# Kernel tuning notes

Measured on AMD Instinct MI355X. Metric: run time of the kernel, lower is better.

Reference implementation:

```python
import jax, jax.numpy as jnp
import numpy as np

G = 2            # num codevector groups
C = 320          # codes per group
VQ_DIM = 256     # codevector_dim
D = VQ_DIM // G  # per-group code dim = 128
TAU = 2.0        # gumbel temperature


def setup_inputs() -> dict:
    key = jax.random.key(0)
    k1, k2, k3, k4, k5, k6 = jax.random.split(key, 6)
    B, T, H = 16, 3072, 512
    x = jax.random.normal(k1, (B, T, H), dtype=jnp.float32)
    masked_token_idx = jax.random.randint(k2, (B, T), 0, 2) > 0  # bool mask
    gumbel_noise = jax.random.gumbel(k3, (B * T * G, C), dtype=jnp.float32)
    q_proj_w = jax.random.normal(k4, (G * C, H), dtype=jnp.float32) * (1.0 / np.sqrt(H))
    q_proj_b = jax.random.normal(k5, (G * C,), dtype=jnp.float32) * 0.02
    codevectors = jax.random.uniform(k6, (1, G * C, D), dtype=jnp.float32)
    return {"x": x, "masked_token_idx": masked_token_idx, "gumbel_noise": gumbel_noise,
            "q_proj_w": q_proj_w, "q_proj_b": q_proj_b, "codevectors": codevectors}


def _perplexity(probs, mask_flat):
    # probs: [B*T, G, C]; masked mean over tokens, then per-codebook perplexity
    m = mask_flat.astype(probs.dtype)
    denom = jnp.maximum(m.sum(), 1.0)
    p = jnp.einsum('ngc,n->gc', probs, m) / denom  # [G, C]
    perp_per_cb = jnp.exp(-jnp.sum(p * jnp.log(p + 1e-7), axis=-1))
    return perp_per_cb.sum()


def reference(x, masked_token_idx, gumbel_noise, q_proj_w, q_proj_b, codevectors):
    B, T, H = x.shape
    N = B * T
    logits = jnp.einsum('bth,kh->btk', x, q_proj_w) + q_proj_b  # [B,T,G*C]
    l = logits.reshape(N * G, C)
    # hard gumbel-softmax with straight-through estimator (training path)
    y_soft = jax.nn.softmax((l + gumbel_noise) / TAU, axis=-1)
    idx = jnp.argmax(y_soft, axis=-1)
    y_hard = jax.nn.one_hot(idx, C, dtype=y_soft.dtype)
    codevector_probs = y_hard + y_soft - jax.lax.stop_gradient(y_soft)  # [N*G, C]
    # perplexity from plain (non-tempered) softmax of logits, over masked tokens
    soft = jax.nn.softmax(l.reshape(N, G, C), axis=-1)
    perplexity = _perplexity(soft, masked_token_idx.reshape(-1))
    # codevector gather-multiply-sum, expressed as a grouped contraction
    # (same math as probs.unsqueeze(-1)*codevectors then sum over codes)
    cv = codevectors.reshape(G, C, D)
    probs3 = codevector_probs.reshape(N, G, C)
    selected = jnp.einsum('ngc,gcd->ngd', probs3, cv).reshape(B, T, G * D)
    return selected, perplexity
```

## Files before the change

kernel.cpp:

```cpp
#include <hip/hip_runtime.h>
#include <hip/hip_bf16.h>
#include <math.h>

#define TOKS 49152
#define HD   512
#define GN   2
#define CN   320
#define DN   128
#define BM   32
#define NTHR 256
#define LSTR 321
#define WSTR 33

#define WS_WELEMS ((size_t)(GN * CN) * HD)
#define WS_W_OFF  4096
#define WS_MID    (WS_W_OFF + 4 * WS_WELEMS)

typedef _Float16 f16x8 __attribute__((ext_vector_type(8)));
typedef float    fx4   __attribute__((ext_vector_type(4)));

__global__ void k_zero(float* pp) {
  int t = threadIdx.x;
  if (t < GN * CN) pp[t] = 0.f;
}

__global__ __launch_bounds__(256) void k_split(const float* __restrict__ src,
                                               _Float16* __restrict__ dh,
                                               _Float16* __restrict__ dl) {
  size_t t    = (size_t)blockIdx.x * 256 + threadIdx.x;
  int    lane = (int)(t & 63);
  size_t blob = t >> 6;
  int    k0   = (int)(blob & 15);
  size_t rb   = blob >> 4;
  const float* p = src + (rb * 16 + (lane & 15)) * HD + k0 * 32 + (lane >> 4) * 8;
  fx4 u = *(const fx4*)p;
  fx4 v = *(const fx4*)(p + 4);
  f16x8 h8, l8;
  #pragma unroll
  for (int e = 0; e < 4; ++e) {
    _Float16 hu = (_Float16)u[e], hv = (_Float16)v[e];
    h8[e]     = hu;
    h8[e + 4] = hv;
    l8[e]     = (_Float16)((u[e] - (float)hu) * 512.f);
    l8[e + 4] = (_Float16)((v[e] - (float)hv) * 512.f);
  }
  *(f16x8*)(dh + t * 8) = h8;
  *(f16x8*)(dl + t * 8) = l8;
}

__global__ __launch_bounds__(NTHR, 2) void k_gemm_ep(
    const float* __restrict__ x, const int* __restrict__ mask,
    const float* __restrict__ gnoise, const float* __restrict__ bias,
    const float* __restrict__ cv, const _Float16* __restrict__ wh,
    const _Float16* __restrict__ wl, float* __restrict__ out,
    float* __restrict__ pp)
{
  __shared__ __align__(16) char smem[46464];
  float* lg   = (float*)smem;
  float* psum = (float*)(smem + 41216);

  const int u   = blockIdx.x;
  const int mt  = ((u >> 4) << 3) | (u & 7);
  const int g   = (u >> 3) & 1;
  const int m0  = mt * BM;
  const int tid = threadIdx.x;
  const int tc  = tid & 63;
  const int tr  = __builtin_amdgcn_readfirstlane(tid >> 6);
  const int l15 = tid & 15;
  const int l4  = (tid & 63) >> 4;

  fx4 aH[2][5], aL[2][5];
  #pragma unroll
  for (int rf = 0; rf < 2; ++rf)
    #pragma unroll
    for (int cf = 0; cf < 5; ++cf) {
      aH[rf][cf] = (fx4){0.f, 0.f, 0.f, 0.f};
      aL[rf][cf] = (fx4){0.f, 0.f, 0.f, 0.f};
    }

  const float* pA0 = x + (size_t)(m0 + l15) * HD + l4 * 8;
  const float* pA1 = pA0 + (size_t)16 * HD;
  const _Float16* pBh[5];
  const _Float16* pBl[5];
  #pragma unroll
  for (int cf = 0; cf < 5; ++cf) {
    const size_t cb = (size_t)(g * 20 + tr * 5 + cf) * 8192 + (size_t)tc * 8;
    pBh[cf] = wh + cb;
    pBl[cf] = wl + cb;
  }

  fx4 x0u_a, x0v_a, x1u_a, x1v_a, x0u_b, x0v_b, x1u_b, x1v_b;
  f16x8 Bh_a[5], Bl_a[5], Bh_b[5], Bl_b[5];
  f16x8 A0h, A0l, A1h, A1l;

#define LOADB(S, K) do {                                                     \
    x0u_##S = *(const fx4*)(pA0 + (size_t)(K) * 32);                         \
    x0v_##S = *(const fx4*)(pA0 + (size_t)(K) * 32 + 4);                     \
    x1u_##S = *(const fx4*)(pA1 + (size_t)(K) * 32);                         \
    x1v_##S = *(const fx4*)(pA1 + (size_t)(K) * 32 + 4);                     \
    _Pragma("unroll")                                                        \
    for (int cf = 0; cf < 5; ++cf) {                                         \
      Bh_##S[cf] = *(const f16x8*)(pBh[cf] + (size_t)(K) * 512);             \
      Bl_##S[cf] = *(const f16x8*)(pBl[cf] + (size_t)(K) * 512);             \
    }                                                                        \
  } while (0)

#define CVT(S) do {                                                          \
    _Pragma("unroll")                                                        \
    for (int e = 0; e < 4; ++e) {                                            \
      _Float16 h; float f;                                                   \
      f = x0u_##S[e]; h = (_Float16)f; A0h[e]   = h;                         \
      A0l[e]   = (_Float16)((f - (float)h) * 512.f);                         \
      f = x0v_##S[e]; h = (_Float16)f; A0h[e+4] = h;                         \
      A0l[e+4] = (_Float16)((f - (float)h) * 512.f);                         \
      f = x1u_##S[e]; h = (_Float16)f; A1h[e]   = h;                         \
      A1l[e]   = (_Float16)((f - (float)h) * 512.f);                         \
      f = x1v_##S[e]; h = (_Float16)f; A1h[e+4] = h;                         \
      A1l[e+4] = (_Float16)((f - (float)h) * 512.f);                         \
    }                                                                        \
  } while (0)

#define MFMAK(S) do {                                                        \
    _Pragma("unroll")                                                        \
    for (int cf = 0; cf < 5; ++cf) {                                         \
      aH[0][cf] = __builtin_amdgcn_mfma_f32_16x16x32_f16(A0h, Bh_##S[cf], aH[0][cf], 0, 0, 0); \
      aH[1][cf] = __builtin_amdgcn_mfma_f32_16x16x32_f16(A1h, Bh_##S[cf], aH[1][cf], 0, 0, 0); \
      aL[0][cf] = __builtin_amdgcn_mfma_f32_16x16x32_f16(A0h, Bl_##S[cf], aL[0][cf], 0, 0, 0); \
      aL[0][cf] = __builtin_amdgcn_mfma_f32_16x16x32_f16(A0l, Bh_##S[cf], aL[0][cf], 0, 0, 0); \
      aL[1][cf] = __builtin_amdgcn_mfma_f32_16x16x32_f16(A1h, Bl_##S[cf], aL[1][cf], 0, 0, 0); \
      aL[1][cf] = __builtin_amdgcn_mfma_f32_16x16x32_f16(A1l, Bh_##S[cf], aL[1][cf], 0, 0, 0); \
    }                                                                        \
  } while (0)

  LOADB(a, 0);
  #pragma unroll 1
  for (int k0 = 0; k0 < 14; k0 += 2) {
    LOADB(b, k0 + 1);
    __builtin_amdgcn_sched_barrier(0);
    CVT(a);
    MFMAK(a);
    LOADB(a, k0 + 2);
    __builtin_amdgcn_sched_barrier(0);
    CVT(b);
    MFMAK(b);
  }
  LOADB(b, 15);
  __builtin_amdgcn_sched_barrier(0);
  CVT(a); MFMAK(a);
  CVT(b); MFMAK(b);
#undef LOADB
#undef CVT
#undef MFMAK

  #pragma unroll
  for (int cf = 0; cf < 5; ++cf) {
    const int col = tr * 80 + cf * 16 + l15;
    const float bc = bias[g * CN + col];
    #pragma unroll
    for (int rf = 0; rf < 2; ++rf)
      #pragma unroll
      for (int e = 0; e < 4; ++e)
        lg[(rf * 16 + l4 * 4 + e) * LSTR + col] =
            aH[rf][cf][e] + aL[rf][cf][e] * (1.f / 512.f) + bc;
  }
  __syncthreads();

  float pacc[5] = {0.f, 0.f, 0.f, 0.f, 0.f};
  #pragma unroll
  for (int i = 0; i < 8; ++i) {
    const int r = tr * 8 + i;
    const int n = m0 + r;
    const size_t grow = ((size_t)n * GN + g) * CN;
    float lv[5], gv[5];
    #pragma unroll
    for (int j = 0; j < 5; ++j) lv[j] = lg[r * LSTR + tc + 64 * j];
    #pragma unroll
    for (int j = 0; j < 5; ++j) gv[j] = gnoise[grow + tc + 64 * j];

    float bv = -3.4e38f; int bi = 1 << 30;
    #pragma unroll
    for (int j = 0; j < 5; ++j) {
      float v = lv[j] + gv[j];
      if (v > bv) { bv = v; bi = tc + 64 * j; }
    }
    for (int off = 1; off < 64; off <<= 1) {
      float ov = __shfl_xor(bv, off);
      int   oi = __shfl_xor(bi, off);
      if (ov > bv || (ov == bv && oi < bi)) { bv = ov; bi = oi; }
    }

    float mx = lv[0];
    #pragma unroll
    for (int j = 1; j < 5; ++j) mx = fmaxf(mx, lv[j]);
    for (int off = 1; off < 64; off <<= 1) mx = fmaxf(mx, __shfl_xor(mx, off));
    float e[5], s = 0.f;
    #pragma unroll
    for (int j = 0; j < 5; ++j) { e[j] = __expf(lv[j] - mx); s += e[j]; }
    for (int off = 1; off < 64; off <<= 1) s += __shfl_xor(s, off);
    const float inv = 1.f / s;
    const float mlt = (mask[n] != 0) ? 1.f : 0.f;
    #pragma unroll
    for (int j = 0; j < 5; ++j) pacc[j] += mlt * e[j] * inv;

    const float2* cvr = (const float2*)(cv + ((size_t)(g * CN + bi)) * DN);
    float2* o2 = (float2*)(out + (size_t)n * (GN * DN) + g * DN);
    o2[tc] = cvr[tc];
  }

  #pragma unroll
  for (int j = 0; j < 5; ++j) psum[tr * CN + tc + 64 * j] = pacc[j];
  __syncthreads();
  for (int c = tid; c < CN; c += NTHR) {
    float s = psum[c] + psum[CN + c] + psum[2 * CN + c] + psum[3 * CN + c];
    atomicAdd(&pp[g * CN + c], s);
  }
}

__global__ __launch_bounds__(NTHR) void k_main_fp32(
    const float* __restrict__ x, const int* __restrict__ mask,
    const float* __restrict__ gnoise, const float* __restrict__ W,
    const float* __restrict__ bias, const float* __restrict__ cv,
    float* __restrict__ out, float* __restrict__ pp)
{
  __shared__ __align__(16) char smem[47360];
  float* w_lds = (float*)smem;
  float* xs    = (float*)(smem + 42240);
  float* lg    = (float*)smem;
  float* psum  = (float*)(smem + 42240);

  const int m0  = blockIdx.x * BM;
  const int g   = blockIdx.y;
  const int tid = threadIdx.x;
  const int tc  = tid & 63;
  const int tr  = tid >> 6;
  const int r0  = tr * 8;

  float acc[8][5];
  #pragma unroll
  for (int i = 0; i < 8; ++i)
    #pragma unroll
    for (int j = 0; j < 5; ++j) acc[i][j] = 0.f;

  const float* Wg = W + (size_t)g * CN * HD;

  for (int k0 = 0; k0 < HD; k0 += 32) {
    __syncthreads();
    #pragma unroll
    for (int t = 0; t < 10; ++t) {
      int idx = tid + t * NTHR;
      int c   = idx >> 3;
      int k4  = idx & 7;
      float4 wv4 = *(const float4*)(Wg + (size_t)c * HD + k0 + k4 * 4);
      float* dst = &w_lds[c * WSTR + k4 * 4];
      dst[0] = wv4.x; dst[1] = wv4.y; dst[2] = wv4.z; dst[3] = wv4.w;
    }
    {
      int r = tid >> 3, k4 = tid & 7;
      float4 xv = *(const float4*)(x + (size_t)(m0 + r) * HD + k0 + k4 * 4);
      float* dst = &xs[r * 32 + k4 * 4];
      dst[0] = xv.x; dst[1] = xv.y; dst[2] = xv.z; dst[3] = xv.w;
    }
    __syncthreads();
    #pragma unroll
    for (int kk = 0; kk < 32; kk += 4) {
      float xq[8][4];
      #pragma unroll
      for (int i = 0; i < 8; ++i) {
        float4 t4 = *(const float4*)&xs[(r0 + i) * 32 + kk];
        xq[i][0] = t4.x; xq[i][1] = t4.y; xq[i][2] = t4.z; xq[i][3] = t4.w;
      }
      #pragma unroll
      for (int q = 0; q < 4; ++q) {
        float wv[5];
        #pragma unroll
        for (int j = 0; j < 5; ++j) wv[j] = w_lds[(tc + 64 * j) * WSTR + kk + q];
        #pragma unroll
        for (int i = 0; i < 8; ++i)
          #pragma unroll
          for (int j = 0; j < 5; ++j)
            acc[i][j] = fmaf(xq[i][q], wv[j], acc[i][j]);
      }
    }
  }
  __syncthreads();

  float bj[5];
  #pragma unroll
  for (int j = 0; j < 5; ++j) bj[j] = bias[g * CN + tc + 64 * j];
  #pragma unroll
  for (int i = 0; i < 8; ++i)
    #pragma unroll
    for (int j = 0; j < 5; ++j)
      lg[(r0 + i) * CN + tc + 64 * j] = acc[i][j] + bj[j];
  __syncthreads();

  float pacc[5] = {0.f, 0.f, 0.f, 0.f, 0.f};
  #pragma unroll
  for (int i = 0; i < 8; ++i) {
    const int r = r0 + i;
    const int n = m0 + r;
    const size_t grow = ((size_t)n * GN + g) * CN;
    float lv[5], gv[5];
    #pragma unroll
    for (int j = 0; j < 5; ++j) lv[j] = lg[r * CN + tc + 64 * j];
    #pragma unroll
    for (int j = 0; j < 5; ++j) gv[j] = gnoise[grow + tc + 64 * j];

    float bv = -3.4e38f; int bi = 1 << 30;
    #pragma unroll
    for (int j = 0; j < 5; ++j) {
      float v = lv[j] + gv[j];
      if (v > bv) { bv = v; bi = tc + 64 * j; }
    }
    for (int off = 1; off < 64; off <<= 1) {
      float ov = __shfl_xor(bv, off);
      int   oi = __shfl_xor(bi, off);
      if (ov > bv || (ov == bv && oi < bi)) { bv = ov; bi = oi; }
    }

    float mx = lv[0];
    #pragma unroll
    for (int j = 1; j < 5; ++j) mx = fmaxf(mx, lv[j]);
    for (int off = 1; off < 64; off <<= 1) mx = fmaxf(mx, __shfl_xor(mx, off));
    float e[5], s = 0.f;
    #pragma unroll
    for (int j = 0; j < 5; ++j) { e[j] = expf(lv[j] - mx); s += e[j]; }
    for (int off = 1; off < 64; off <<= 1) s += __shfl_xor(s, off);
    const float inv = 1.f / s;
    const float mlt = (mask[n] != 0) ? 1.f : 0.f;
    #pragma unroll
    for (int j = 0; j < 5; ++j) pacc[j] += mlt * e[j] * inv;

    const float2* cvr = (const float2*)(cv + ((size_t)(g * CN + bi)) * DN);
    float2* o2 = (float2*)(out + (size_t)n * (GN * DN) + g * DN);
    o2[tc] = cvr[tc];
  }

  #pragma unroll
  for (int j = 0; j < 5; ++j) psum[tr * CN + tc + 64 * j] = pacc[j];
  __syncthreads();
  for (int c = tid; c < CN; c += NTHR) {
    float s = psum[c] + psum[CN + c] + psum[2 * CN + c] + psum[3 * CN + c];
    atomicAdd(&pp[g * CN + c], s);
  }
}

__global__ __launch_bounds__(640) void k_final(
    const float* __restrict__ pp, const int* __restrict__ mask,
    float* __restrict__ out, int out_off)
{
  __shared__ float red[10];
  __shared__ float eL[GN * CN];
  __shared__ float perp_parts[GN];
  const int tid = threadIdx.x;

  float cnt = 0.f;
  for (int i = tid; i < TOKS; i += 640) cnt += (mask[i] != 0) ? 1.f : 0.f;
  for (int off = 1; off < 64; off <<= 1) cnt += __shfl_xor(cnt, off);
  if ((tid & 63) == 0) red[tid >> 6] = cnt;
  __syncthreads();
  float denom = 0.f;
  #pragma unroll
  for (int w = 0; w < 10; ++w) denom += red[w];
  denom = fmaxf(denom, 1.f);

  const float p = pp[tid] / denom;
  eL[tid] = p * logf(p + 1e-7f);
  __syncthreads();

  if (tid < 2 * 64) {
    const int gg = tid >> 6, ll = tid & 63;
    float s = 0.f;
    #pragma unroll
    for (int j = 0; j < 5; ++j) s += eL[gg * CN + ll + 64 * j];
    for (int off = 1; off < 64; off <<= 1) s += __shfl_xor(s, off);
    if (ll == 0) perp_parts[gg] = expf(-s);
  }
  __syncthreads();
  if (tid == 0) out[out_off] = perp_parts[0] + perp_parts[1];
}

extern "C" void kernel_launch(void* const* d_in, const int* in_sizes, int n_in,
                              void* d_out, int out_size, void* d_ws, size_t ws_size,
                              hipStream_t stream) {
  const float* x     = (const float*)d_in[0];
  const int*   mask  = (const int*)d_in[1];
  const float* gn    = (const float*)d_in[2];
  const float* W     = (const float*)d_in[3];
  const float* bias  = (const float*)d_in[4];
  const float* cv    = (const float*)d_in[5];
  float* out = (float*)d_out;
  float* pp  = (float*)d_ws;

  hipLaunchKernelGGL(k_zero, dim3(1), dim3(640), 0, stream, pp);

  if (ws_size >= WS_MID) {
    _Float16* wh = (_Float16*)((char*)d_ws + WS_W_OFF);
    _Float16* wl = wh + WS_WELEMS;
    hipLaunchKernelGGL(k_split, dim3((int)(WS_WELEMS / 8 / 256)), dim3(256), 0,
                       stream, W, wh, wl);
    hipLaunchKernelGGL(k_gemm_ep, dim3(TOKS / BM * GN), dim3(NTHR), 0, stream,
                       x, mask, gn, bias, cv, wh, wl, out, pp);
  } else {
    hipLaunchKernelGGL(k_main_fp32, dim3(TOKS / BM, GN), dim3(NTHR), 0, stream,
                       x, mask, gn, W, bias, cv, out, pp);
  }

  hipLaunchKernelGGL(k_final, dim3(1), dim3(640), 0, stream,
                     pp, mask, out, out_size - 1);
}
```

Before: 242.2 us.

## Stage GEMM tiles in LDS with 64-row blocks and async global-to-LDS loads

The fused GEMM+epilogue kernel moves from 32-row tiles with 4 waves to 64-row tiles with 8 waves. The split fp16 weight tiles are staged into shared memory via global_load_lds, and the x tile goes through an LDS buffer, so each wave no longer loads its own B fragments straight from global memory. B data is shared across two row-waves, cutting weight traffic per output row. The epilogue now runs in two 32-row passes that reuse the logits buffer, and the perplexity-accumulator zeroing is folded into the split kernel to drop one launch. The cost is extra syncthreads per k-step and no software prefetch across k-steps.

```diff
diff --git a/kernel.cpp b/kernel.cpp
--- a/kernel.cpp
+++ b/kernel.cpp
@@ -7,9 +7,16 @@
 #define GN   2
 #define CN   320
 #define DN   128
-#define BM   32
-#define NTHR 256
+#define BM   64
+#define NTHR 512
 #define LSTR 321
+#define ASTR 36
+#define SB_L 20480
+#define SA   40960
+#define SMEM_SZ 51328
+
+#define BMF  32
+#define NTHRF 256
 #define WSTR 33
 
 #define WS_WELEMS ((size_t)(GN * CN) * HD)
@@ -19,6 +26,22 @@
 typedef _Float16 f16x8 __attribute__((ext_vector_type(8)));
 typedef float    fx4   __attribute__((ext_vector_type(4)));
 
+#define GLD_LDS16(gp, lp)                                                    \
+  __builtin_amdgcn_global_load_lds(                                          \
+      (const __attribute__((address_space(1))) void*)(gp),                   \
+      (__attribute__((address_space(3))) void*)(lp), 16, 0, 0)
+
+#define CVT8(U, V, HH, LL) do {                                              \
+    _Pragma("unroll")                                                        \
+    for (int e = 0; e < 4; ++e) {                                            \
+      _Float16 h;                                                            \
+      h = (_Float16)U[e]; HH[e] = h;                                         \
+      LL[e] = (_Float16)((U[e] - (float)h) * 512.f);                         \
+      h = (_Float16)V[e]; HH[e + 4] = h;                                     \
+      LL[e + 4] = (_Float16)((V[e] - (float)h) * 512.f);                     \
+    }                                                                        \
+  } while (0)
+
 __global__ void k_zero(float* pp) {
   int t = threadIdx.x;
   if (t < GN * CN) pp[t] = 0.f;
@@ -26,7 +49,12 @@
 
 __global__ __launch_bounds__(256) void k_split(const float* __restrict__ src,
                                                _Float16* __restrict__ dh,
-                                               _Float16* __restrict__ dl) {
+                                               _Float16* __restrict__ dl,
+                                               float* __restrict__ pp) {
+  if (blockIdx.x < 3) {
+    int i = blockIdx.x * 256 + threadIdx.x;
+    if (i < GN * CN) pp[i] = 0.f;
+  }
   size_t t    = (size_t)blockIdx.x * 256 + threadIdx.x;
   int    lane = (int)(t & 63);
   size_t blob = t >> 6;
@@ -48,16 +76,17 @@
   *(f16x8*)(dl + t * 8) = l8;
 }
 
-__global__ __launch_bounds__(NTHR, 2) void k_gemm_ep(
+__global__ __launch_bounds__(NTHR, 4) void k_gemm_ep(
     const float* __restrict__ x, const int* __restrict__ mask,
     const float* __restrict__ gnoise, const float* __restrict__ bias,
     const float* __restrict__ cv, const _Float16* __restrict__ wh,
     const _Float16* __restrict__ wl, float* __restrict__ out,
     float* __restrict__ pp)
 {
-  __shared__ __align__(16) char smem[46464];
+  __shared__ __align__(16) char smem[SMEM_SZ];
+  float* As   = (float*)(smem + SA);
   float* lg   = (float*)smem;
-  float* psum = (float*)(smem + 41216);
+  float* psum = (float*)(smem + 41088);
 
   const int u   = blockIdx.x;
   const int mt  = ((u >> 4) << 3) | (u & 7);
@@ -65,9 +94,11 @@
   const int m0  = mt * BM;
   const int tid = threadIdx.x;
   const int tc  = tid & 63;
-  const int tr  = __builtin_amdgcn_readfirstlane(tid >> 6);
+  const int w   = tid >> 6;
+  const int wr  = w >> 2;
+  const int wc  = w & 3;
   const int l15 = tid & 15;
-  const int l4  = (tid & 63) >> 4;
+  const int l4  = tc >> 4;
 
   fx4 aH[2][5], aL[2][5];
   #pragma unroll
@@ -78,145 +109,122 @@
       aL[rf][cf] = (fx4){0.f, 0.f, 0.f, 0.f};
     }
 
-  const float* pA0 = x + (size_t)(m0 + l15) * HD + l4 * 8;
-  const float* pA1 = pA0 + (size_t)16 * HD;
-  const _Float16* pBh[5];
-  const _Float16* pBl[5];
-  #pragma unroll
-  for (int cf = 0; cf < 5; ++cf) {
-    const size_t cb = (size_t)(g * 20 + tr * 5 + cf) * 8192 + (size_t)tc * 8;
-    pBh[cf] = wh + cb;
-    pBl[cf] = wl + cb;
-  }
-
-  fx4 x0u_a, x0v_a, x1u_a, x1v_a, x0u_b, x0v_b, x1u_b, x1v_b;
-  f16x8 Bh_a[5], Bl_a[5], Bh_b[5], Bl_b[5];
-  f16x8 A0h, A0l, A1h, A1l;
-
-#define LOADB(S, K) do {                                                     \
-    x0u_##S = *(const fx4*)(pA0 + (size_t)(K) * 32);                         \
-    x0v_##S = *(const fx4*)(pA0 + (size_t)(K) * 32 + 4);                     \
-    x1u_##S = *(const fx4*)(pA1 + (size_t)(K) * 32);                         \
-    x1v_##S = *(const fx4*)(pA1 + (size_t)(K) * 32 + 4);                     \
-    _Pragma("unroll")                                                        \
-    for (int cf = 0; cf < 5; ++cf) {                                         \
-      Bh_##S[cf] = *(const f16x8*)(pBh[cf] + (size_t)(K) * 512);             \
-      Bl_##S[cf] = *(const f16x8*)(pBl[cf] + (size_t)(K) * 512);             \
-    }                                                                        \
-  } while (0)
-
-#define CVT(S) do {                                                          \
-    _Pragma("unroll")                                                        \
-    for (int e = 0; e < 4; ++e) {                                            \
-      _Float16 h; float f;                                                   \
-      f = x0u_##S[e]; h = (_Float16)f; A0h[e]   = h;                         \
-      A0l[e]   = (_Float16)((f - (float)h) * 512.f);                         \
-      f = x0v_##S[e]; h = (_Float16)f; A0h[e+4] = h;                         \
-      A0l[e+4] = (_Float16)((f - (float)h) * 512.f);                         \
-      f = x1u_##S[e]; h = (_Float16)f; A1h[e]   = h;                         \
-      A1l[e]   = (_Float16)((f - (float)h) * 512.f);                         \
-      f = x1v_##S[e]; h = (_Float16)f; A1h[e+4] = h;                         \
-      A1l[e+4] = (_Float16)((f - (float)h) * 512.f);                         \
-    }                                                                        \
-  } while (0)
-
-#define MFMAK(S) do {                                                        \
-    _Pragma("unroll")                                                        \
-    for (int cf = 0; cf < 5; ++cf) {                                         \
-      aH[0][cf] = __builtin_amdgcn_mfma_f32_16x16x32_f16(A0h, Bh_##S[cf], aH[0][cf], 0, 0, 0); \
-      aH[1][cf] = __builtin_amdgcn_mfma_f32_16x16x32_f16(A1h, Bh_##S[cf], aH[1][cf], 0, 0, 0); \
-      aL[0][cf] = __builtin_amdgcn_mfma_f32_16x16x32_f16(A0h, Bl_##S[cf], aL[0][cf], 0, 0, 0); \
-      aL[0][cf] = __builtin_amdgcn_mfma_f32_16x16x32_f16(A0l, Bh_##S[cf], aL[0][cf], 0, 0, 0); \
-      aL[1][cf] = __builtin_amdgcn_mfma_f32_16x16x32_f16(A1h, Bl_##S[cf], aL[1][cf], 0, 0, 0); \
-      aL[1][cf] = __builtin_amdgcn_mfma_f32_16x16x32_f16(A1l, Bh_##S[cf], aL[1][cf], 0, 0, 0); \
-    }                                                                        \
-  } while (0)
-
-  LOADB(a, 0);
+  const _Float16* bb = (w < 4) ? wh : wl;
+  const int cb0      = (w < 4) ? w * 5 : w * 5 - 20;
+  const _Float16* bsrc = bb + (size_t)(g * 20 + cb0) * 8192 + (size_t)tc * 8;
+  char* bdst = smem + (size_t)(w * 5) * 1024;
+  const int ar = w * 8 + (tc >> 3);
+  const int ac = tc & 7;
+  const float* asrc = x + (size_t)(m0 + ar) * HD + ac * 4;
+  float* adst = &As[ar * ASTR + ac * 4];
+
   #pragma unroll 1
-  for (int k0 = 0; k0 < 14; k0 += 2) {
-    LOADB(b, k0 + 1);
-    __builtin_amdgcn_sched_barrier(0);
-    CVT(a);
-    MFMAK(a);
-    LOADB(a, k0 + 2);
-    __builtin_amdgcn_sched_barrier(0);
-    CVT(b);
-    MFMAK(b);
-  }
-  LOADB(b, 15);
-  __builtin_amdgcn_sched_barrier(0);
-  CVT(a); MFMAK(a);
-  CVT(b); MFMAK(b);
-#undef LOADB
-#undef CVT
-#undef MFMAK
-
-  #pragma unroll
-  for (int cf = 0; cf < 5; ++cf) {
-    const int col = tr * 80 + cf * 16 + l15;
-    const float bc = bias[g * CN + col];
-    #pragma unroll
-    for (int rf = 0; rf < 2; ++rf)
-      #pragma unroll
-      for (int e = 0; e < 4; ++e)
-        lg[(rf * 16 + l4 * 4 + e) * LSTR + col] =
-            aH[rf][cf][e] + aL[rf][cf][e] * (1.f / 512.f) + bc;
-  }
-  __syncthreads();
+  for (int t = 0; t < 16; ++t) {
+    __syncthreads();
+    fx4 av = *(const fx4*)(asrc + t * 32);
+    #pragma unroll
+    for (int q = 0; q < 5; ++q)
+      GLD_LDS16(bsrc + (size_t)q * 8192 + (size_t)t * 512, bdst + q * 1024);
+    *(fx4*)adst = av;
+    __syncthreads();
+
+    const float* a0p = &As[(wr * 32 + l15) * ASTR + l4 * 8];
+    fx4 u0 = *(const fx4*)a0p;
+    fx4 v0 = *(const fx4*)(a0p + 4);
+    fx4 u1 = *(const fx4*)(a0p + 16 * ASTR);
+    fx4 v1 = *(const fx4*)(a0p + 16 * ASTR + 4);
+    f16x8 A0h, A0l, A1h, A1l;
+    CVT8(u0, v0, A0h, A0l);
+    CVT8(u1, v1, A1h, A1l);
+    #pragma unroll
+    for (int cf = 0; cf < 5; ++cf) {
+      f16x8 Bh = *(const f16x8*)(smem + (wc * 5 + cf) * 1024 + tc * 16);
+      f16x8 Bl = *(const f16x8*)(smem + SB_L + (wc * 5 + cf) * 1024 + tc * 16);
+      aH[0][cf] = __builtin_amdgcn_mfma_f32_16x16x32_f16(A0h, Bh, aH[0][cf], 0, 0, 0);
+      aH[1][cf] = __builtin_amdgcn_mfma_f32_16x16x32_f16(A1h, Bh, aH[1][cf], 0, 0, 0);
+      aL[0][cf] = __builtin_amdgcn_mfma_f32_16x16x32_f16(A0h, Bl, aL[0][cf], 0, 0, 0);
+      aL[0][cf] = __builtin_amdgcn_mfma_f32_16x16x32_f16(A0l, Bh, aL[0][cf], 0, 0, 0);
+      aL[1][cf] = __builtin_amdgcn_mfma_f32_16x16x32_f16(A1h, Bl, aL[1][cf], 0, 0, 0);
+      aL[1][cf] = __builtin_amdgcn_mfma_f32_16x16x32_f16(A1l, Bh, aL[1][cf], 0, 0, 0);
+    }
+  }
+  __syncthreads();
+
+  float bj[5];
+  #pragma unroll
+  for (int cf = 0; cf < 5; ++cf) bj[cf] = bias[g * CN + wc * 80 + cf * 16 + l15];
 
   float pacc[5] = {0.f, 0.f, 0.f, 0.f, 0.f};
   #pragma unroll
-  for (int i = 0; i < 8; ++i) {
-    const int r = tr * 8 + i;
-    const int n = m0 + r;
-    const size_t grow = ((size_t)n * GN + g) * CN;
-    float lv[5], gv[5];
-    #pragma unroll
-    for (int j = 0; j < 5; ++j) lv[j] = lg[r * LSTR + tc + 64 * j];
-    #pragma unroll
-    for (int j = 0; j < 5; ++j) gv[j] = gnoise[grow + tc + 64 * j];
-
-    float bv = -3.4e38f; int bi = 1 << 30;
-    #pragma unroll
-    for (int j = 0; j < 5; ++j) {
-      float v = lv[j] + gv[j];
-      if (v > bv) { bv = v; bi = tc + 64 * j; }
-    }
-    for (int off = 1; off < 64; off <<= 1) {
-      float ov = __shfl_xor(bv, off);
-      int   oi = __shfl_xor(bi, off);
-      if (ov > bv || (ov == bv && oi < bi)) { bv = ov; bi = oi; }
-    }
-
-    float mx = lv[0];
-    #pragma unroll
-    for (int j = 1; j < 5; ++j) mx = fmaxf(mx, lv[j]);
-    for (int off = 1; off < 64; off <<= 1) mx = fmaxf(mx, __shfl_xor(mx, off));
-    float e[5], s = 0.f;
-    #pragma unroll
-    for (int j = 0; j < 5; ++j) { e[j] = __expf(lv[j] - mx); s += e[j]; }
-    for (int off = 1; off < 64; off <<= 1) s += __shfl_xor(s, off);
-    const float inv = 1.f / s;
-    const float mlt = (mask[n] != 0) ? 1.f : 0.f;
-    #pragma unroll
-    for (int j = 0; j < 5; ++j) pacc[j] += mlt * e[j] * inv;
-
-    const float2* cvr = (const float2*)(cv + ((size_t)(g * CN + bi)) * DN);
-    float2* o2 = (float2*)(out + (size_t)n * (GN * DN) + g * DN);
-    o2[tc] = cvr[tc];
-  }
-
-  #pragma unroll
-  for (int j = 0; j < 5; ++j) psum[tr * CN + tc + 64 * j] = pacc[j];
+  for (int p = 0; p < 2; ++p) {
+    if (wr == p) {
+      #pragma unroll
+      for (int cf = 0; cf < 5; ++cf) {
+        const int col = wc * 80 + cf * 16 + l15;
+        #pragma unroll
+        for (int rf = 0; rf < 2; ++rf)
+          #pragma unroll
+          for (int e = 0; e < 4; ++e)
+            lg[(rf * 16 + l4 * 4 + e) * LSTR + col] =
+                aH[rf][cf][e] + aL[rf][cf][e] * (1.f / 512.f) + bj[cf];
+      }
+    }
+    __syncthreads();
+    #pragma unroll
+    for (int i = 0; i < 4; ++i) {
+      const int rl = w * 4 + i;
+      const int n  = m0 + p * 32 + rl;
+      const size_t grow = ((size_t)n * GN + g) * CN;
+      float lv[5], gv[5];
+      #pragma unroll
+      for (int j = 0; j < 5; ++j) lv[j] = lg[rl * LSTR + tc + 64 * j];
+      #pragma unroll
+      for (int j = 0; j < 5; ++j) gv[j] = gnoise[grow + tc + 64 * j];
+
+      float bv = -3.4e38f; int bi = 1 << 30;
+      #pragma unroll
+      for (int j = 0; j < 5; ++j) {
+        float v = lv[j] + gv[j];
+        if (v > bv) { bv = v; bi = tc + 64 * j; }
+      }
+      for (int off = 1; off < 64; off <<= 1) {
+        float ov = __shfl_xor(bv, off);
+        int   oi = __shfl_xor(bi, off);
+        if (ov > bv || (ov == bv && oi < bi)) { bv = ov; bi = oi; }
+      }
+
+      float mx = lv[0];
+      #pragma unroll
+      for (int j = 1; j < 5; ++j) mx = fmaxf(mx, lv[j]);
+      for (int off = 1; off < 64; off <<= 1) mx = fmaxf(mx, __shfl_xor(mx, off));
+      float e[5], s = 0.f;
+      #pragma unroll
+      for (int j = 0; j < 5; ++j) { e[j] = __expf(lv[j] - mx); s += e[j]; }
+      for (int off = 1; off < 64; off <<= 1) s += __shfl_xor(s, off);
+      const float inv = 1.f / s;
+      const float mlt = (mask[n] != 0) ? 1.f : 0.f;
+      #pragma unroll
+      for (int j = 0; j < 5; ++j) pacc[j] += mlt * e[j] * inv;
+
+      const float2* cvr = (const float2*)(cv + ((size_t)(g * CN + bi)) * DN);
+      float2* o2 = (float2*)(out + (size_t)n * (GN * DN) + g * DN);
+      o2[tc] = cvr[tc];
+    }
+    __syncthreads();
+  }
+
+  #pragma unroll
+  for (int j = 0; j < 5; ++j) psum[w * CN + tc + 64 * j] = pacc[j];
   __syncthreads();
   for (int c = tid; c < CN; c += NTHR) {
-    float s = psum[c] + psum[CN + c] + psum[2 * CN + c] + psum[3 * CN + c];
+    float s = 0.f;
+    #pragma unroll
+    for (int q = 0; q < 8; ++q) s += psum[q * CN + c];
     atomicAdd(&pp[g * CN + c], s);
   }
 }
 
-__global__ __launch_bounds__(NTHR) void k_main_fp32(
+__global__ __launch_bounds__(NTHRF) void k_main_fp32(
     const float* __restrict__ x, const int* __restrict__ mask,
     const float* __restrict__ gnoise, const float* __restrict__ W,
     const float* __restrict__ bias, const float* __restrict__ cv,
@@ -228,7 +236,7 @@
   float* lg    = (float*)smem;
   float* psum  = (float*)(smem + 42240);
 
-  const int m0  = blockIdx.x * BM;
+  const int m0  = blockIdx.x * BMF;
   const int g   = blockIdx.y;
   const int tid = threadIdx.x;
   const int tc  = tid & 63;
@@ -247,7 +255,7 @@
     __syncthreads();
     #pragma unroll
     for (int t = 0; t < 10; ++t) {
-      int idx = tid + t * NTHR;
+      int idx = tid + t * NTHRF;
       int c   = idx >> 3;
       int k4  = idx & 7;
       float4 wv4 = *(const float4*)(Wg + (size_t)c * HD + k0 + k4 * 4);
@@ -339,7 +347,7 @@
   #pragma unroll
   for (int j = 0; j < 5; ++j) psum[tr * CN + tc + 64 * j] = pacc[j];
   __syncthreads();
-  for (int c = tid; c < CN; c += NTHR) {
+  for (int c = tid; c < CN; c += NTHRF) {
     float s = psum[c] + psum[CN + c] + psum[2 * CN + c] + psum[3 * CN + c];
     atomicAdd(&pp[g * CN + c], s);
   }
@@ -392,17 +400,16 @@
   float* out = (float*)d_out;
   float* pp  = (float*)d_ws;
 
-  hipLaunchKernelGGL(k_zero, dim3(1), dim3(640), 0, stream, pp);
-
   if (ws_size >= WS_MID) {
     _Float16* wh = (_Float16*)((char*)d_ws + WS_W_OFF);
     _Float16* wl = wh + WS_WELEMS;
     hipLaunchKernelGGL(k_split, dim3((int)(WS_WELEMS / 8 / 256)), dim3(256), 0,
-                       stream, W, wh, wl);
+                       stream, W, wh, wl, pp);
     hipLaunchKernelGGL(k_gemm_ep, dim3(TOKS / BM * GN), dim3(NTHR), 0, stream,
                        x, mask, gn, bias, cv, wh, wl, out, pp);
   } else {
-    hipLaunchKernelGGL(k_main_fp32, dim3(TOKS / BM, GN), dim3(NTHR), 0, stream,
+    hipLaunchKernelGGL(k_zero, dim3(1), dim3(640), 0, stream, pp);
+    hipLaunchKernelGGL(k_main_fp32, dim3(TOKS / BMF, GN), dim3(NTHRF), 0, stream,
                        x, mask, gn, W, bias, cv, out, pp);
   }
 
```

Result: faster. 208.2 us (-14.0%).
